# Performance work log

Measured on AMD Instinct MI355X. Metric: run time of the kernel, lower is better.

The kernel has to match this reference:

```python
import jax, jax.numpy as jnp
import numpy as np

N_NODES = 50000
N_EDGES = 1200000
IN_FEATS = 64
OUT_FEATS = 64
NEG_SLOPE = 0.01  # F.leaky_relu default


def setup_inputs() -> dict:
    key = jax.random.key(0)
    k1, k2, k3, k4, k5, k6 = jax.random.split(key, 6)
    feature = jax.random.normal(k1, (N_NODES, IN_FEATS), dtype=jnp.float32)
    attn_w = jax.random.normal(k2, (2 * IN_FEATS, 1), dtype=jnp.float32) * 0.1
    lin_w = jax.random.normal(k3, (OUT_FEATS, 2 * IN_FEATS), dtype=jnp.float32) * 0.1
    lin_b = jax.random.normal(k4, (OUT_FEATS,), dtype=jnp.float32) * 0.1
    src = jax.random.randint(k5, (N_EDGES,), 0, N_NODES, dtype=jnp.int32)
    dst = jax.random.randint(k6, (N_EDGES,), 0, N_NODES, dtype=jnp.int32)
    return {"feature": feature, "attn_w": attn_w, "lin_w": lin_w,
            "lin_b": lin_b, "src": src, "dst": dst}


def reference(feature, attn_w, lin_w, lin_b, src, dst):
    N = feature.shape[0]
    # edge attention: leaky_relu(attn_fc([h_src, h_dst]))
    # split attn weight to avoid materializing the [E, 2*in] concat
    a_src, a_dst = attn_w[:IN_FEATS, 0], attn_w[IN_FEATS:, 0]
    e = jax.nn.leaky_relu(feature[src] @ a_src + feature[dst] @ a_dst,
                          negative_slope=NEG_SLOPE)  # [E]
    # segment softmax over incoming edges of each destination node
    emax = jax.ops.segment_max(e, dst, num_segments=N)
    emax = jnp.where(jnp.isfinite(emax), emax, 0.0)  # guard empty segments
    ex = jnp.exp(e - emax[dst])                       # [E]
    denom = jax.ops.segment_sum(ex, dst, num_segments=N)          # [N]
    num = jax.ops.segment_sum(ex[:, None] * feature[src], dst,
                              num_segments=N)                      # [N, in]
    hm = jnp.where(denom[:, None] > 0, num / denom[:, None], 0.0)
    # node apply: relu(Linear([h, hm]))
    h = jnp.concatenate([feature, hm], axis=1) @ lin_w.T + lin_b
    return jax.nn.relu(h)
```

## Files before the change

kernel.cpp:

```cpp
#include <hip/hip_runtime.h>
#include <math.h>

#define N_NODES 50000
#define N_EDGES 1200000
#define F 64
#define CAP 49
#define OVF_MAX 1024
#define NBIN 196
#define BSTR 16
#define CAP_BIN 7680
#define TILE 8192
#define NTILE ((N_EDGES + TILE - 1) / TILE)

typedef __attribute__((ext_vector_type(8))) short short8;
typedef __attribute__((ext_vector_type(4))) float v4f;


__device__ __forceinline__ unsigned short f32_to_bf16_rne(float f) {
    unsigned u = __float_as_uint(f);
    return (unsigned short)((u + 0x7FFFu + ((u >> 16) & 1u)) >> 16);
}
__device__ __forceinline__ float bf16_to_f32(unsigned short u) {
    return __uint_as_float(((unsigned)u) << 16);
}

__global__ void k_prep(const float* __restrict__ feature,
                       const float* __restrict__ attn_w,
                       float* __restrict__ s, float* __restrict__ dd,
                       int* __restrict__ bin_cnt, int* __restrict__ ovf_cnt,
                       unsigned short* __restrict__ fb) {
    int gid = blockIdx.x * blockDim.x + threadIdx.x;
    if (gid < NBIN * BSTR) bin_cnt[gid] = 0;
    if (gid == NBIN * BSTR) *ovf_cnt = 0;
    int wave = gid >> 6;
    int lane = threadIdx.x & 63;
    if (wave >= N_NODES) return;
    float f = feature[wave * F + lane];
    fb[wave * F + lane] = f32_to_bf16_rne(f);
    float sv = f * attn_w[lane];
    float dv = f * attn_w[F + lane];
    #pragma unroll
    for (int o = 32; o > 0; o >>= 1) {
        sv += __shfl_down(sv, o, 64);
        dv += __shfl_down(dv, o, 64);
    }
    if (lane == 0) {
        s[wave] = sv;
        dd[wave] = dv;
    }
}

__global__ __launch_bounds__(256) void k_bin(
        const int* __restrict__ src, const int* __restrict__ dst,
        int* __restrict__ bin_cnt, unsigned* __restrict__ binned) {
    __shared__ unsigned ord[TILE];
    __shared__ int cnt_l[NBIN], off_l[NBIN], cur_l[NBIN], base_g[NBIN];
    __shared__ int buf[256];
    int t = threadIdx.x;
    int e0 = blockIdx.x * TILE;
    int ecnt = N_EDGES - e0; if (ecnt > TILE) ecnt = TILE;
    for (int i = t; i < NBIN; i += 256) cnt_l[i] = 0;
    __syncthreads();
    int n4 = ecnt >> 2;
    const int4* s4p = (const int4*)src + (e0 >> 2);
    const int4* d4p = (const int4*)dst + (e0 >> 2);
    for (int c = t; c < n4; c += 256) {
        int4 d4 = d4p[c];
        atomicAdd(&cnt_l[d4.x >> 8], 1);
        atomicAdd(&cnt_l[d4.y >> 8], 1);
        atomicAdd(&cnt_l[d4.z >> 8], 1);
        atomicAdd(&cnt_l[d4.w >> 8], 1);
    }
    __syncthreads();
    int v0 = (t < NBIN) ? cnt_l[t] : 0;
    buf[t] = v0;
    __syncthreads();
    #pragma unroll
    for (int d = 1; d < 256; d <<= 1) {
        int x = (t >= d) ? buf[t - d] : 0;
        __syncthreads();
        buf[t] += x;
        __syncthreads();
    }
    if (t < NBIN) {
        int off = buf[t] - v0;
        off_l[t] = off;
        cur_l[t] = off;
        base_g[t] = atomicAdd(&bin_cnt[t * BSTR], v0);
    }
    __syncthreads();
    for (int c = t; c < n4; c += 256) {
        int4 d4 = d4p[c];
        int4 s4 = s4p[c];
        int dv[4] = {d4.x, d4.y, d4.z, d4.w};
        int sv[4] = {s4.x, s4.y, s4.z, s4.w};
        #pragma unroll
        for (int u = 0; u < 4; u++) {
            int r = atomicAdd(&cur_l[dv[u] >> 8], 1);
            ord[r] = (((unsigned)dv[u]) << 16) | (unsigned)sv[u];
        }
    }
    __syncthreads();
    for (int i = t; i < ecnt; i += 256) {
        unsigned v = ord[i];
        int b = v >> 24;
        int pos = base_g[b] + (i - off_l[b]);
        if (pos < CAP_BIN) binned[(size_t)b * CAP_BIN + pos] = v;
    }
}

__global__ __launch_bounds__(256) void k_bucket(
        const unsigned* __restrict__ binned, const int* __restrict__ bin_cnt,
        int* __restrict__ cnt, unsigned short* __restrict__ bucket,
        int* __restrict__ ovf_cnt, unsigned* __restrict__ ovf) {
    __shared__ int cnt_l[256];
    __shared__ __align__(16) unsigned short buck_l[256 * CAP];
    int bin = blockIdx.x;
    int t = threadIdx.x;
    int n0 = bin << 8;
    int nn = N_NODES - n0; if (nn > 256) nn = 256;
    cnt_l[t] = 0;
    __syncthreads();
    int E = bin_cnt[bin * BSTR];
    if (E > CAP_BIN) E = CAP_BIN;
    const unsigned* be = binned + (size_t)bin * CAP_BIN;
    for (int i = t; i < E; i += 256) {
        unsigned v = be[i];
        int local = (v >> 16) & 255;
        int sid = (int)(v & 0xFFFFu);
        int r = atomicAdd(&cnt_l[local], 1);
        if (r < CAP) {
            buck_l[local * CAP + r] = (unsigned short)sid;
        } else {
            int o = atomicAdd(ovf_cnt, 1);
            if (o < OVF_MAX)
                ovf[o] = ((unsigned)(n0 + local) << 16) | (unsigned)sid;
        }
    }
    __syncthreads();
    if (t < nn) cnt[n0 + t] = cnt_l[t];
    int nu4 = (nn * CAP * 2) >> 4;
    const uint4* bl4 = (const uint4*)buck_l;
    uint4* bg4 = (uint4*)(bucket + (size_t)n0 * CAP);
    for (int i = t; i < nu4; i += 256) bg4[i] = bl4[i];
}

__global__ __launch_bounds__(512) void k_aggregate(
        const unsigned short* __restrict__ bucket,
        const int* __restrict__ cnt,
        const float* __restrict__ s, const float* __restrict__ dd,
        const unsigned short* __restrict__ fb,
        float* __restrict__ out) {
    int t = threadIdx.x;
    int wid = t >> 6, lane = t & 63;
    int n = blockIdx.x * 8 + wid;
    int deg = cnt[n];
    if (deg > CAP) return;
    if (deg == 0) { out[n * F + lane] = 0.0f; return; }
    int si = 0;
    float ev = -1e30f;
    if (lane < deg) {
        si = (int)bucket[n * CAP + lane];
        float v = s[si] + dd[n];
        ev = v > 0.0f ? v : 0.01f * v;
    }
    float m = ev;
    #pragma unroll
    for (int o = 32; o > 0; o >>= 1)
        m = fmaxf(m, __shfl_xor(m, o, 64));
    float p = (lane < deg) ? __expf(ev - m) : 0.0f;
    float l = p;
    #pragma unroll
    for (int o = 32; o > 0; o >>= 1)
        l += __shfl_xor(l, o, 64);
    p *= __builtin_amdgcn_rcpf(l);

    int grp = lane >> 4;
    int c16 = lane & 15;
    const ushort4* f4 = (const ushort4*)fb;
    ushort4 fv0[8], fv1[8];
    #pragma unroll
    for (int u = 0; u < 8; u++) {
        int sk = __shfl(si, u * 4 + grp, 64);
        fv0[u] = f4[sk * 16 + c16];
    }
    bool two = deg > 32;
    if (two) {
        #pragma unroll
        for (int u = 0; u < 8; u++) {
            int sk = __shfl(si, 32 + u * 4 + grp, 64);
            fv1[u] = f4[sk * 16 + c16];
        }
    }
    float a0 = 0.0f, a1 = 0.0f, a2 = 0.0f, a3 = 0.0f;
    #pragma unroll
    for (int u = 0; u < 8; u++) {
        float pw = __shfl(p, u * 4 + grp, 64);
        a0 = fmaf(pw, bf16_to_f32(fv0[u].x), a0);
        a1 = fmaf(pw, bf16_to_f32(fv0[u].y), a1);
        a2 = fmaf(pw, bf16_to_f32(fv0[u].z), a2);
        a3 = fmaf(pw, bf16_to_f32(fv0[u].w), a3);
    }
    if (two) {
        #pragma unroll
        for (int u = 0; u < 8; u++) {
            float pw = __shfl(p, 32 + u * 4 + grp, 64);
            a0 = fmaf(pw, bf16_to_f32(fv1[u].x), a0);
            a1 = fmaf(pw, bf16_to_f32(fv1[u].y), a1);
            a2 = fmaf(pw, bf16_to_f32(fv1[u].z), a2);
            a3 = fmaf(pw, bf16_to_f32(fv1[u].w), a3);
        }
    }
    a0 += __shfl_xor(a0, 16, 64); a0 += __shfl_xor(a0, 32, 64);
    a1 += __shfl_xor(a1, 16, 64); a1 += __shfl_xor(a1, 32, 64);
    a2 += __shfl_xor(a2, 16, 64); a2 += __shfl_xor(a2, 32, 64);
    a3 += __shfl_xor(a3, 16, 64); a3 += __shfl_xor(a3, 32, 64);
    if (lane < 16) {
        v4f st = {a0, a1, a2, a3};
        ((v4f*)out)[n * 16 + c16] = st;
    }
}

__global__ __launch_bounds__(256) void k_cleanup(
        const unsigned short* __restrict__ bucket,
        const int* __restrict__ cnt,
        const int* __restrict__ ovf_cnt, const unsigned int* __restrict__ ovf,
        const float* __restrict__ s, const float* __restrict__ dd,
        const float* __restrict__ feature,
        float* __restrict__ out) {
    int M = *ovf_cnt;
    if (M > OVF_MAX) M = OVF_MAX;
    if (M == 0) return;
    __shared__ int list[128];
    __shared__ int nlist;
    __shared__ unsigned short edg[4][256];
    int t = threadIdx.x;
    if (t == 0) {
        nlist = 0;
        for (int i = 0; i < M; i++) {
            int d = (int)(ovf[i] >> 16);
            bool seen = false;
            for (int j = 0; j < nlist; j++) if (list[j] == d) seen = true;
            if (!seen && nlist < 128) list[nlist++] = d;
        }
    }
    __syncthreads();
    int wid = t >> 6, lane = t & 63;
    for (int idx = wid; idx < nlist; idx += 4) {
        int n = list[idx];
        int deg = cnt[n];
        if (lane < CAP) edg[wid][lane] = bucket[n * CAP + lane];
        int k2 = CAP;
        for (int base = 0; base < M; base += 64) {
            int i2 = base + lane;
            unsigned val = 0;
            bool mt = false;
            if (i2 < M) { val = ovf[i2]; mt = ((int)(val >> 16) == n); }
            unsigned long long mask = __ballot(mt);
            if (mt) {
                int pos = k2 + __popcll(mask & ((1ULL << lane) - 1ULL));
                if (pos < 256) edg[wid][pos] = (unsigned short)(val & 0xFFFFu);
            }
            k2 += __popcll(mask);
        }
        __threadfence_block();
        int nd = deg < 256 ? deg : 256;
        float m = -1e30f, l = 0.0f, acc = 0.0f;
        float dn = dd[n];
        for (int c0 = 0; c0 < nd; c0 += 64) {
            int j = c0 + lane;
            int sid = 0;
            float ev = -1e30f;
            if (j < nd) {
                sid = (int)edg[wid][j];
                float v = s[sid] + dn;
                ev = v > 0.0f ? v : 0.01f * v;
            }
            float cm = ev;
            #pragma unroll
            for (int o = 32; o > 0; o >>= 1)
                cm = fmaxf(cm, __shfl_xor(cm, o, 64));
            float np = (j < nd) ? __expf(ev - cm) : 0.0f;
            float cl = np;
            #pragma unroll
            for (int o = 32; o > 0; o >>= 1)
                cl += __shfl_xor(cl, o, 64);
            float cacc = 0.0f;
            int c = nd - c0; if (c > 64) c = 64;
            for (int k = 0; k < c; k += 16) {
                float fvv[16];
                #pragma unroll
                for (int u = 0; u < 16; u++) {
                    int sk = __builtin_amdgcn_readlane(sid, k + u);
                    fvv[u] = feature[sk * F + lane];
                }
                #pragma unroll
                for (int u = 0; u < 16; u++) {
                    float pk = __uint_as_float(
                        __builtin_amdgcn_readlane(__float_as_uint(np), k + u));
                    cacc = fmaf(pk, fvv[u], cacc);
                }
            }
            float mn = fmaxf(m, cm);
            float sc = __expf(m - mn);
            float sc2 = __expf(cm - mn);
            l = l * sc + cl * sc2;
            acc = acc * sc + cacc * sc2;
            m = mn;
        }
        out[n * F + lane] = acc / l;
    }
}

__global__ __launch_bounds__(256) void k_proj(
        const unsigned short* __restrict__ fb,
        const float* __restrict__ lin_w, const float* __restrict__ lin_b,
        float* __restrict__ out) {
    __shared__ unsigned short Wl[64 * 136];
    int t = threadIdx.x;
    for (int i = t; i < 64 * 128; i += 256)
        Wl[(i >> 7) * 136 + (i & 127)] = f32_to_bf16_rne(lin_w[i]);
    __syncthreads();
    int wid = t >> 6, lane = t & 63;
    int wgl = blockIdx.x * 4 + wid;
    int n0 = wgl * 16;
    if (n0 >= N_NODES) return;
    int m = lane & 15, quad = lane >> 4;
    short8 afr[4];
    #pragma unroll
    for (int ks = 0; ks < 2; ks++) {
        int kb = ks * 32 + quad * 8;
        afr[ks] = *(const short8*)&fb[(size_t)(n0 + m) * F + kb];
    }
    #pragma unroll
    for (int ks = 2; ks < 4; ks++) {
        int kb = ks * 32 + quad * 8 - 64;
        const float* sp = out + (size_t)(n0 + m) * F + kb;
        float4 x0 = ((const float4*)sp)[0];
        float4 x1 = ((const float4*)sp)[1];
        short8 a;
        a[0] = (short)f32_to_bf16_rne(x0.x);
        a[1] = (short)f32_to_bf16_rne(x0.y);
        a[2] = (short)f32_to_bf16_rne(x0.z);
        a[3] = (short)f32_to_bf16_rne(x0.w);
        a[4] = (short)f32_to_bf16_rne(x1.x);
        a[5] = (short)f32_to_bf16_rne(x1.y);
        a[6] = (short)f32_to_bf16_rne(x1.z);
        a[7] = (short)f32_to_bf16_rne(x1.w);
        afr[ks] = a;
    }
    #pragma unroll
    for (int nt = 0; nt < 4; nt++) {
        v4f acc = {0.0f, 0.0f, 0.0f, 0.0f};
        #pragma unroll
        for (int ks = 0; ks < 4; ks++) {
            int kb = ks * 32 + quad * 8;
            short8 b = *(const short8*)&Wl[(nt * 16 + m) * 136 + kb];
            acc = __builtin_amdgcn_mfma_f32_16x16x32_bf16(afr[ks], b, acc,
                                                          0, 0, 0);
        }
        int colo = nt * 16 + m;
        float bias = lin_b[colo];
        #pragma unroll
        for (int r = 0; r < 4; r++) {
            int row = quad * 4 + r;
            float v = acc[r] + bias;
            out[(size_t)(n0 + row) * F + colo] = fmaxf(v, 0.0f);
        }
    }
}

extern "C" void kernel_launch(void* const* d_in, const int* in_sizes, int n_in,
                              void* d_out, int out_size, void* d_ws, size_t ws_size,
                              hipStream_t stream) {
    const float* feature = (const float*)d_in[0];
    const float* attn_w  = (const float*)d_in[1];
    const float* lin_w   = (const float*)d_in[2];
    const float* lin_b   = (const float*)d_in[3];
    const int*   src     = (const int*)d_in[4];
    const int*   dst     = (const int*)d_in[5];
    float* out = (float*)d_out;
    char* ws = (char*)d_ws;

    float*          s       = (float*)(ws);
    float*          dd      = (float*)(ws + 200000);
    int*            cnt     = (int*)  (ws + 400000);
    int*            bin_cnt = (int*)  (ws + 600000);
    int*            ovf_cnt = (int*)  (ws + 612544);
    unsigned*       ovf     = (unsigned*)(ws + 612608);
    unsigned short* bucket  = (unsigned short*)(ws + 616704);
    unsigned*       binned  = (unsigned*)(ws + 5516704);
    unsigned short* fb      = (unsigned short*)(ws + 11537824);

    k_prep<<<(N_NODES * 64) / 256, 256, 0, stream>>>(
        feature, attn_w, s, dd, bin_cnt, ovf_cnt, fb);
    k_bin<<<NTILE, 256, 0, stream>>>(src, dst, bin_cnt, binned);
    k_bucket<<<NBIN, 256, 0, stream>>>(
        binned, bin_cnt, cnt, bucket, ovf_cnt, ovf);
    k_aggregate<<<N_NODES / 8, 512, 0, stream>>>(
        bucket, cnt, s, dd, fb, out);
    k_cleanup<<<1, 256, 0, stream>>>(
        bucket, cnt, ovf_cnt, ovf, s, dd, feature, out);
    k_proj<<<(3125 + 3) / 4, 256, 0, stream>>>(fb, lin_w, lin_b, out);
}
```

Before: 148.0 us.

## Fuse bucketing, aggregation and projection into one per-64-node kernel

Shrinks bins from 256 to 64 nodes (782 bins), then fuses bucket construction, softmax aggregation and the MFMA projection into a single kernel per bin. Bucket lists stay in LDS and aggregated rows go to an LDS tile, so the bucket array is no longer written and read back and the intermediate hm no longer round-trips through global memory. Two kernel launches are removed. Overflow nodes are now projected inside the cleanup kernel with an fp32 dot product. The cost is fewer, heavier blocks (782 blocks, each looping 16 nodes per wave serially), which reduces parallelism and latency hiding for the gather loads, plus a per-block reload of lin_w into LDS.

```diff
diff --git a/kernel.cpp b/kernel.cpp
--- a/kernel.cpp
+++ b/kernel.cpp
@@ -6,9 +6,9 @@
 #define F 64
 #define CAP 49
 #define OVF_MAX 1024
-#define NBIN 196
+#define NBIN 782
 #define BSTR 16
-#define CAP_BIN 7680
+#define CAP_BIN 2304
 #define TILE 8192
 #define NTILE ((N_EDGES + TILE - 1) / TILE)
 
@@ -66,14 +66,21 @@
     const int4* d4p = (const int4*)dst + (e0 >> 2);
     for (int c = t; c < n4; c += 256) {
         int4 d4 = d4p[c];
-        atomicAdd(&cnt_l[d4.x >> 8], 1);
-        atomicAdd(&cnt_l[d4.y >> 8], 1);
-        atomicAdd(&cnt_l[d4.z >> 8], 1);
-        atomicAdd(&cnt_l[d4.w >> 8], 1);
-    }
-    __syncthreads();
-    int v0 = (t < NBIN) ? cnt_l[t] : 0;
-    buf[t] = v0;
+        atomicAdd(&cnt_l[d4.x >> 6], 1);
+        atomicAdd(&cnt_l[d4.y >> 6], 1);
+        atomicAdd(&cnt_l[d4.z >> 6], 1);
+        atomicAdd(&cnt_l[d4.w >> 6], 1);
+    }
+    __syncthreads();
+    int c0[4];
+    int sum = 0;
+    #pragma unroll
+    for (int j = 0; j < 4; j++) {
+        int idx = t * 4 + j;
+        c0[j] = (idx < NBIN) ? cnt_l[idx] : 0;
+        sum += c0[j];
+    }
+    buf[t] = sum;
     __syncthreads();
     #pragma unroll
     for (int d = 1; d < 256; d <<= 1) {
@@ -82,11 +89,16 @@
         buf[t] += x;
         __syncthreads();
     }
-    if (t < NBIN) {
-        int off = buf[t] - v0;
-        off_l[t] = off;
-        cur_l[t] = off;
-        base_g[t] = atomicAdd(&bin_cnt[t * BSTR], v0);
+    int excl = buf[t] - sum;
+    #pragma unroll
+    for (int j = 0; j < 4; j++) {
+        int idx = t * 4 + j;
+        if (idx < NBIN) {
+            off_l[idx] = excl;
+            cur_l[idx] = excl;
+            base_g[idx] = atomicAdd(&bin_cnt[idx * BSTR], c0[j]);
+        }
+        excl += c0[j];
     }
     __syncthreads();
     for (int c = t; c < n4; c += 256) {
@@ -96,37 +108,46 @@
         int sv[4] = {s4.x, s4.y, s4.z, s4.w};
         #pragma unroll
         for (int u = 0; u < 4; u++) {
-            int r = atomicAdd(&cur_l[dv[u] >> 8], 1);
+            int r = atomicAdd(&cur_l[dv[u] >> 6], 1);
             ord[r] = (((unsigned)dv[u]) << 16) | (unsigned)sv[u];
         }
     }
     __syncthreads();
     for (int i = t; i < ecnt; i += 256) {
         unsigned v = ord[i];
-        int b = v >> 24;
+        int b = v >> 22;
         int pos = base_g[b] + (i - off_l[b]);
         if (pos < CAP_BIN) binned[(size_t)b * CAP_BIN + pos] = v;
     }
 }
 
-__global__ __launch_bounds__(256) void k_bucket(
+__global__ __launch_bounds__(256) void k_fused(
         const unsigned* __restrict__ binned, const int* __restrict__ bin_cnt,
         int* __restrict__ cnt, unsigned short* __restrict__ bucket,
-        int* __restrict__ ovf_cnt, unsigned* __restrict__ ovf) {
-    __shared__ int cnt_l[256];
-    __shared__ __align__(16) unsigned short buck_l[256 * CAP];
+        int* __restrict__ ovf_cnt, unsigned* __restrict__ ovf,
+        const float* __restrict__ s, const float* __restrict__ dd,
+        const unsigned short* __restrict__ fb,
+        const float* __restrict__ lin_w, const float* __restrict__ lin_b,
+        float* __restrict__ out) {
+    __shared__ int cnt_l[64];
+    __shared__ unsigned short buck_l[64 * CAP];
+    __shared__ unsigned short Wl[64 * 136];
+    __shared__ float xl[4][16][64];
+    int t = threadIdx.x;
+    int wid = t >> 6, lane = t & 63;
     int bin = blockIdx.x;
-    int t = threadIdx.x;
-    int n0 = bin << 8;
-    int nn = N_NODES - n0; if (nn > 256) nn = 256;
-    cnt_l[t] = 0;
+    int n0 = bin << 6;
+    int nn = N_NODES - n0; if (nn > 64) nn = 64;
+    for (int i = t; i < 64 * 128; i += 256)
+        Wl[(i >> 7) * 136 + (i & 127)] = f32_to_bf16_rne(lin_w[i]);
+    if (t < 64) cnt_l[t] = 0;
     __syncthreads();
     int E = bin_cnt[bin * BSTR];
     if (E > CAP_BIN) E = CAP_BIN;
     const unsigned* be = binned + (size_t)bin * CAP_BIN;
     for (int i = t; i < E; i += 256) {
         unsigned v = be[i];
-        int local = (v >> 16) & 255;
+        int local = (v >> 16) & 63;
         int sid = (int)(v & 0xFFFFu);
         int r = atomicAdd(&cnt_l[local], 1);
         if (r < CAP) {
@@ -138,86 +159,131 @@
         }
     }
     __syncthreads();
-    if (t < nn) cnt[n0 + t] = cnt_l[t];
-    int nu4 = (nn * CAP * 2) >> 4;
-    const uint4* bl4 = (const uint4*)buck_l;
-    uint4* bg4 = (uint4*)(bucket + (size_t)n0 * CAP);
-    for (int i = t; i < nu4; i += 256) bg4[i] = bl4[i];
-}
-
-__global__ __launch_bounds__(512) void k_aggregate(
-        const unsigned short* __restrict__ bucket,
-        const int* __restrict__ cnt,
-        const float* __restrict__ s, const float* __restrict__ dd,
-        const unsigned short* __restrict__ fb,
-        float* __restrict__ out) {
-    int t = threadIdx.x;
-    int wid = t >> 6, lane = t & 63;
-    int n = blockIdx.x * 8 + wid;
-    int deg = cnt[n];
-    if (deg > CAP) return;
-    if (deg == 0) { out[n * F + lane] = 0.0f; return; }
-    int si = 0;
-    float ev = -1e30f;
-    if (lane < deg) {
-        si = (int)bucket[n * CAP + lane];
-        float v = s[si] + dd[n];
-        ev = v > 0.0f ? v : 0.01f * v;
-    }
-    float m = ev;
-    #pragma unroll
-    for (int o = 32; o > 0; o >>= 1)
-        m = fmaxf(m, __shfl_xor(m, o, 64));
-    float p = (lane < deg) ? __expf(ev - m) : 0.0f;
-    float l = p;
-    #pragma unroll
-    for (int o = 32; o > 0; o >>= 1)
-        l += __shfl_xor(l, o, 64);
-    p *= __builtin_amdgcn_rcpf(l);
-
-    int grp = lane >> 4;
-    int c16 = lane & 15;
+    if (t < nn) {
+        cnt[n0 + t] = cnt_l[t];
+        if (cnt_l[t] > CAP) {
+            for (int k2 = 0; k2 < CAP; k2++)
+                bucket[(size_t)(n0 + t) * CAP + k2] = buck_l[t * CAP + k2];
+        }
+    }
+    __syncthreads();
     const ushort4* f4 = (const ushort4*)fb;
-    ushort4 fv0[8], fv1[8];
-    #pragma unroll
-    for (int u = 0; u < 8; u++) {
-        int sk = __shfl(si, u * 4 + grp, 64);
-        fv0[u] = f4[sk * 16 + c16];
-    }
-    bool two = deg > 32;
-    if (two) {
+    for (int j = 0; j < 16; j++) {
+        int local = wid * 16 + j;
+        if (local >= nn) break;
+        int deg = cnt_l[local];
+        if (deg == 0 || deg > CAP) {
+            if (lane < 16) {
+                v4f z = {0.0f, 0.0f, 0.0f, 0.0f};
+                ((v4f*)&xl[wid][j][0])[lane] = z;
+            }
+            continue;
+        }
+        int si = 0;
+        float ev = -1e30f;
+        if (lane < deg) {
+            si = (int)buck_l[local * CAP + lane];
+            float v = s[si] + dd[n0 + local];
+            ev = v > 0.0f ? v : 0.01f * v;
+        }
+        float m = ev;
+        #pragma unroll
+        for (int o = 32; o > 0; o >>= 1)
+            m = fmaxf(m, __shfl_xor(m, o, 64));
+        float p = (lane < deg) ? __expf(ev - m) : 0.0f;
+        float l = p;
+        #pragma unroll
+        for (int o = 32; o > 0; o >>= 1)
+            l += __shfl_xor(l, o, 64);
+        p *= __builtin_amdgcn_rcpf(l);
+        int grp = lane >> 4;
+        int c16 = lane & 15;
+        ushort4 fv0[8], fv1[8];
         #pragma unroll
         for (int u = 0; u < 8; u++) {
-            int sk = __shfl(si, 32 + u * 4 + grp, 64);
-            fv1[u] = f4[sk * 16 + c16];
-        }
-    }
-    float a0 = 0.0f, a1 = 0.0f, a2 = 0.0f, a3 = 0.0f;
-    #pragma unroll
-    for (int u = 0; u < 8; u++) {
-        float pw = __shfl(p, u * 4 + grp, 64);
-        a0 = fmaf(pw, bf16_to_f32(fv0[u].x), a0);
-        a1 = fmaf(pw, bf16_to_f32(fv0[u].y), a1);
-        a2 = fmaf(pw, bf16_to_f32(fv0[u].z), a2);
-        a3 = fmaf(pw, bf16_to_f32(fv0[u].w), a3);
-    }
-    if (two) {
+            int sk = __shfl(si, u * 4 + grp, 64);
+            fv0[u] = f4[sk * 16 + c16];
+        }
+        bool two = deg > 32;
+        if (two) {
+            #pragma unroll
+            for (int u = 0; u < 8; u++) {
+                int sk = __shfl(si, 32 + u * 4 + grp, 64);
+                fv1[u] = f4[sk * 16 + c16];
+            }
+        }
+        float a0 = 0.0f, a1 = 0.0f, a2 = 0.0f, a3 = 0.0f;
         #pragma unroll
         for (int u = 0; u < 8; u++) {
-            float pw = __shfl(p, 32 + u * 4 + grp, 64);
-            a0 = fmaf(pw, bf16_to_f32(fv1[u].x), a0);
-            a1 = fmaf(pw, bf16_to_f32(fv1[u].y), a1);
-            a2 = fmaf(pw, bf16_to_f32(fv1[u].z), a2);
-            a3 = fmaf(pw, bf16_to_f32(fv1[u].w), a3);
-        }
-    }
-    a0 += __shfl_xor(a0, 16, 64); a0 += __shfl_xor(a0, 32, 64);
-    a1 += __shfl_xor(a1, 16, 64); a1 += __shfl_xor(a1, 32, 64);
-    a2 += __shfl_xor(a2, 16, 64); a2 += __shfl_xor(a2, 32, 64);
-    a3 += __shfl_xor(a3, 16, 64); a3 += __shfl_xor(a3, 32, 64);
-    if (lane < 16) {
-        v4f st = {a0, a1, a2, a3};
-        ((v4f*)out)[n * 16 + c16] = st;
+            float pw = __shfl(p, u * 4 + grp, 64);
+            a0 = fmaf(pw, bf16_to_f32(fv0[u].x), a0);
+            a1 = fmaf(pw, bf16_to_f32(fv0[u].y), a1);
+            a2 = fmaf(pw, bf16_to_f32(fv0[u].z), a2);
+            a3 = fmaf(pw, bf16_to_f32(fv0[u].w), a3);
+        }
+        if (two) {
+            #pragma unroll
+            for (int u = 0; u < 8; u++) {
+                float pw = __shfl(p, 32 + u * 4 + grp, 64);
+                a0 = fmaf(pw, bf16_to_f32(fv1[u].x), a0);
+                a1 = fmaf(pw, bf16_to_f32(fv1[u].y), a1);
+                a2 = fmaf(pw, bf16_to_f32(fv1[u].z), a2);
+                a3 = fmaf(pw, bf16_to_f32(fv1[u].w), a3);
+            }
+        }
+        a0 += __shfl_xor(a0, 16, 64); a0 += __shfl_xor(a0, 32, 64);
+        a1 += __shfl_xor(a1, 16, 64); a1 += __shfl_xor(a1, 32, 64);
+        a2 += __shfl_xor(a2, 16, 64); a2 += __shfl_xor(a2, 32, 64);
+        a3 += __shfl_xor(a3, 16, 64); a3 += __shfl_xor(a3, 32, 64);
+        if (lane < 16) {
+            v4f st = {a0, a1, a2, a3};
+            ((v4f*)&xl[wid][j][0])[c16] = st;
+        }
+    }
+    int n0w = n0 + wid * 16;
+    if (n0w >= N_NODES) return;
+    int m = lane & 15, quad = lane >> 4;
+    short8 afr[4];
+    #pragma unroll
+    for (int ks = 0; ks < 2; ks++) {
+        int kb = ks * 32 + quad * 8;
+        afr[ks] = *(const short8*)&fb[(size_t)(n0w + m) * F + kb];
+    }
+    #pragma unroll
+    for (int ks = 2; ks < 4; ks++) {
+        int kb = ks * 32 + quad * 8 - 64;
+        const float* sp = &xl[wid][m][kb];
+        float4 x0 = ((const float4*)sp)[0];
+        float4 x1 = ((const float4*)sp)[1];
+        short8 a;
+        a[0] = (short)f32_to_bf16_rne(x0.x);
+        a[1] = (short)f32_to_bf16_rne(x0.y);
+        a[2] = (short)f32_to_bf16_rne(x0.z);
+        a[3] = (short)f32_to_bf16_rne(x0.w);
+        a[4] = (short)f32_to_bf16_rne(x1.x);
+        a[5] = (short)f32_to_bf16_rne(x1.y);
+        a[6] = (short)f32_to_bf16_rne(x1.z);
+        a[7] = (short)f32_to_bf16_rne(x1.w);
+        afr[ks] = a;
+    }
+    #pragma unroll
+    for (int nt = 0; nt < 4; nt++) {
+        v4f acc = {0.0f, 0.0f, 0.0f, 0.0f};
+        #pragma unroll
+        for (int ks = 0; ks < 4; ks++) {
+            int kb = ks * 32 + quad * 8;
+            short8 b = *(const short8*)&Wl[(nt * 16 + m) * 136 + kb];
+            acc = __builtin_amdgcn_mfma_f32_16x16x32_bf16(afr[ks], b, acc,
+                                                          0, 0, 0);
+        }
+        int colo = nt * 16 + m;
+        float bias = lin_b[colo];
+        #pragma unroll
+        for (int r = 0; r < 4; r++) {
+            int row = quad * 4 + r;
+            float v = acc[r] + bias;
+            out[(size_t)(n0w + row) * F + colo] = fmaxf(v, 0.0f);
+        }
     }
 }
 
@@ -227,14 +293,19 @@
         const int* __restrict__ ovf_cnt, const unsigned int* __restrict__ ovf,
         const float* __restrict__ s, const float* __restrict__ dd,
         const float* __restrict__ feature,
+        const float* __restrict__ lin_w, const float* __restrict__ lin_b,
         float* __restrict__ out) {
     int M = *ovf_cnt;
     if (M > OVF_MAX) M = OVF_MAX;
     if (M == 0) return;
+    __shared__ float Wl[64 * 129];
     __shared__ int list[128];
     __shared__ int nlist;
     __shared__ unsigned short edg[4][256];
+    __shared__ float xc[4][128];
     int t = threadIdx.x;
+    for (int i = t; i < 64 * 128; i += 256)
+        Wl[(i >> 7) * 129 + (i & 127)] = lin_w[i];
     if (t == 0) {
         nlist = 0;
         for (int i = 0; i < M; i++) {
@@ -308,65 +379,15 @@
             acc = acc * sc + cacc * sc2;
             m = mn;
         }
-        out[n * F + lane] = acc / l;
-    }
-}
-
-__global__ __launch_bounds__(256) void k_proj(
-        const unsigned short* __restrict__ fb,
-        const float* __restrict__ lin_w, const float* __restrict__ lin_b,
-        float* __restrict__ out) {
-    __shared__ unsigned short Wl[64 * 136];
-    int t = threadIdx.x;
-    for (int i = t; i < 64 * 128; i += 256)
-        Wl[(i >> 7) * 136 + (i & 127)] = f32_to_bf16_rne(lin_w[i]);
-    __syncthreads();
-    int wid = t >> 6, lane = t & 63;
-    int wgl = blockIdx.x * 4 + wid;
-    int n0 = wgl * 16;
-    if (n0 >= N_NODES) return;
-    int m = lane & 15, quad = lane >> 4;
-    short8 afr[4];
-    #pragma unroll
-    for (int ks = 0; ks < 2; ks++) {
-        int kb = ks * 32 + quad * 8;
-        afr[ks] = *(const short8*)&fb[(size_t)(n0 + m) * F + kb];
-    }
-    #pragma unroll
-    for (int ks = 2; ks < 4; ks++) {
-        int kb = ks * 32 + quad * 8 - 64;
-        const float* sp = out + (size_t)(n0 + m) * F + kb;
-        float4 x0 = ((const float4*)sp)[0];
-        float4 x1 = ((const float4*)sp)[1];
-        short8 a;
-        a[0] = (short)f32_to_bf16_rne(x0.x);
-        a[1] = (short)f32_to_bf16_rne(x0.y);
-        a[2] = (short)f32_to_bf16_rne(x0.z);
-        a[3] = (short)f32_to_bf16_rne(x0.w);
-        a[4] = (short)f32_to_bf16_rne(x1.x);
-        a[5] = (short)f32_to_bf16_rne(x1.y);
-        a[6] = (short)f32_to_bf16_rne(x1.z);
-        a[7] = (short)f32_to_bf16_rne(x1.w);
-        afr[ks] = a;
-    }
-    #pragma unroll
-    for (int nt = 0; nt < 4; nt++) {
-        v4f acc = {0.0f, 0.0f, 0.0f, 0.0f};
-        #pragma unroll
-        for (int ks = 0; ks < 4; ks++) {
-            int kb = ks * 32 + quad * 8;
-            short8 b = *(const short8*)&Wl[(nt * 16 + m) * 136 + kb];
-            acc = __builtin_amdgcn_mfma_f32_16x16x32_bf16(afr[ks], b, acc,
-                                                          0, 0, 0);
-        }
-        int colo = nt * 16 + m;
-        float bias = lin_b[colo];
-        #pragma unroll
-        for (int r = 0; r < 4; r++) {
-            int row = quad * 4 + r;
-            float v = acc[r] + bias;
-            out[(size_t)(n0 + row) * F + colo] = fmaxf(v, 0.0f);
-        }
+        float hm = acc / l;
+        xc[wid][lane] = feature[n * F + lane];
+        xc[wid][64 + lane] = hm;
+        __threadfence_block();
+        float oa = lin_b[lane];
+        #pragma unroll
+        for (int k = 0; k < 128; k++)
+            oa += xc[wid][k] * Wl[lane * 129 + k];
+        out[n * F + lane] = fmaxf(oa, 0.0f);
     }
 }
 
@@ -386,20 +407,18 @@
     float*          dd      = (float*)(ws + 200000);
     int*            cnt     = (int*)  (ws + 400000);
     int*            bin_cnt = (int*)  (ws + 600000);
-    int*            ovf_cnt = (int*)  (ws + 612544);
-    unsigned*       ovf     = (unsigned*)(ws + 612608);
-    unsigned short* bucket  = (unsigned short*)(ws + 616704);
-    unsigned*       binned  = (unsigned*)(ws + 5516704);
-    unsigned short* fb      = (unsigned short*)(ws + 11537824);
+    int*            ovf_cnt = (int*)  (ws + 650048);
+    unsigned*       ovf     = (unsigned*)(ws + 650112);
+    unsigned short* bucket  = (unsigned short*)(ws + 654208);
+    unsigned*       binned  = (unsigned*)(ws + 5554208);
+    unsigned short* fb      = (unsigned short*)(ws + 12761120);
 
     k_prep<<<(N_NODES * 64) / 256, 256, 0, stream>>>(
         feature, attn_w, s, dd, bin_cnt, ovf_cnt, fb);
     k_bin<<<NTILE, 256, 0, stream>>>(src, dst, bin_cnt, binned);
-    k_bucket<<<NBIN, 256, 0, stream>>>(
-        binned, bin_cnt, cnt, bucket, ovf_cnt, ovf);
-    k_aggregate<<<N_NODES / 8, 512, 0, stream>>>(
-        bucket, cnt, s, dd, fb, out);
+    k_fused<<<NBIN, 256, 0, stream>>>(
+        binned, bin_cnt, cnt, bucket, ovf_cnt, ovf, s, dd, fb,
+        lin_w, lin_b, out);
     k_cleanup<<<1, 256, 0, stream>>>(
-        bucket, cnt, ovf_cnt, ovf, s, dd, feature, out);
-    k_proj<<<(3125 + 3) / 4, 256, 0, stream>>>(fb, lin_w, lin_b, out);
-}
+        bucket, cnt, ovf_cnt, ovf, s, dd, feature, lin_w, lin_b, out);
+}
```

Result: faster. 143.1 us (-3.3%).
